# Performance work log

Measured on AMD Instinct MI355X. Metric: run time of the kernel, lower is better.

## Reference

```python
import jax, jax.numpy as jnp
import numpy as np

TEMPERATURE = 0.5
EPS = 1e-12  # torch F.normalize eps


def setup_inputs() -> dict:
    key = jax.random.key(0)
    k1, k2 = jax.random.split(key)
    z_i = jax.random.normal(k1, (32, 128, 128), dtype=jnp.float32)
    z_j = jax.random.normal(k2, (32, 128, 128), dtype=jnp.float32)
    return {"z_i": z_i, "z_j": z_j}


def _l2_normalize(x):
    # matches torch F.normalize(dim=1): x / max(||x||, eps)
    n = jnp.sqrt(jnp.sum(x * x, axis=1, keepdims=True))
    return x / jnp.maximum(n, EPS)


def _off_diagonal(a):
    # rows of a with the diagonal removed, row-major order -> [n, n-1]
    n = a.shape[0]
    return a.reshape(-1)[:-1].reshape(n - 1, n + 1)[:, 1:].reshape(n, n - 1)


def reference(z_i, z_j):
    B, S, D = z_i.shape
    N = B * S
    zi = _l2_normalize(z_i.reshape(N, D))
    zj = _l2_normalize(z_j.reshape(N, D))
    r = jnp.concatenate([zi, zj], axis=0)              # [2N, D]
    sim = r @ r.T                                      # [2N, 2N]
    # positives: off-diagonals at +/-N (unaffected by the diag -inf fill)
    pos = jnp.concatenate([jnp.diagonal(sim, N), jnp.diagonal(sim, -N)])  # [2N]
    # negatives: all non-diagonal entries, row-major (== torch boolean-mask view)
    neg = _off_diagonal(sim)                           # [2N, 2N-1]
    logits = jnp.concatenate([pos[:, None], neg], axis=1) / TEMPERATURE  # [2N, 2N]
    # labels are all 0 -> CE(sum) / 2N == mean of -log_softmax[:, 0]
    loss = -jax.nn.log_softmax(logits, axis=1)[:, 0]
    return jnp.sum(loss) / (2 * N)
```

## Files before the change

### kernel.cpp

```cpp
#include <hip/hip_runtime.h>
#include <hip/hip_bf16.h>
#include <math.h>

#define NPAIR 4096
#define D 128
#define TWO_N 8192
#define NJC 8
#define NPART (NJC * 2)

typedef short bf16x8 __attribute__((ext_vector_type(8)));
typedef float f32x4 __attribute__((ext_vector_type(4)));

__device__ __forceinline__ void async_ld16(void* lds, const void* g) {
    __builtin_amdgcn_global_load_lds(
        (__attribute__((address_space(1))) const unsigned int*)g,
        (__attribute__((address_space(3))) unsigned int*)lds, 16, 0, 0);
}

__device__ inline unsigned short f2bf(float x) {
    union { float f; unsigned u; } v; v.f = x;
    unsigned u = v.u;
    unsigned r = u + 0x7fffu + ((u >> 16) & 1u);
    return (unsigned short)(r >> 16);
}

__global__ __launch_bounds__(256) void norm_kernel(const float* __restrict__ zi,
                                                   const float* __restrict__ zj,
                                                   unsigned int* __restrict__ Rb,
                                                   float* __restrict__ pos,
                                                   float* __restrict__ out) {
    if (blockIdx.x == 0 && threadIdx.x == 0) out[0] = 0.f;
    int k = blockIdx.x * 4 + (threadIdx.x >> 6);
    int t = threadIdx.x & 63;
    const float2 a = *(const float2*)(zi + k * D + 2 * t);
    const float2 b = *(const float2*)(zj + k * D + 2 * t);
    float si = a.x * a.x + a.y * a.y;
    float sj = b.x * b.x + b.y * b.y;
    float dt = a.x * b.x + a.y * b.y;
    #pragma unroll
    for (int m = 1; m < 64; m <<= 1) {
        si += __shfl_xor(si, m, 64);
        sj += __shfl_xor(sj, m, 64);
        dt += __shfl_xor(dt, m, 64);
    }
    float ii = 1.0f / fmaxf(sqrtf(si), 1e-12f);
    float ij = 1.0f / fmaxf(sqrtf(sj), 1e-12f);
    unsigned short b0 = f2bf(a.x * ii), b1 = f2bf(a.y * ii);
    Rb[k * (D / 2) + t] = (unsigned)b0 | ((unsigned)b1 << 16);
    b0 = f2bf(b.x * ij); b1 = f2bf(b.y * ij);
    Rb[(k + NPAIR) * (D / 2) + t] = (unsigned)b0 | ((unsigned)b1 << 16);
    if (t == 0) pos[k] = dt * ii * ij;
}

__global__ __launch_bounds__(256, 2) void simexp_kernel(const uint4* __restrict__ Rb,
                                                        float* __restrict__ rspart) {
    __shared__ uint4 Bs[2][2048];
    const int bi = blockIdx.x >> 3, jc = blockIdx.x & 7;
    const int tid = threadIdx.x;
    const int wave = tid >> 6, lane = tid & 63;
    const int rp = lane & 15, q = lane >> 4;
    const int wr = (wave & 1) * 64;
    const int wc = (wave >> 1) * 64;

    bf16x8 afr[4][4];
    {
        const uint4* Ab = Rb + (bi * 128 + wr + rp) * 16;
        #pragma unroll
        for (int kt = 0; kt < 4; ++kt)
            #pragma unroll
            for (int rt = 0; rt < 4; ++rt)
                afr[kt][rt] = *(const bf16x8*)&Ab[rt * 256 + kt * 4 + q];
    }

    const int rl15 = wave * 4 + q;
    const int laneoff = rl15 * 256 + ((rp ^ rl15) << 4);
    const char* Rbb = (const char*)Rb;

    float rs[16];
    #pragma unroll
    for (int i = 0; i < 16; ++i) rs[i] = 0.f;

    {
        const char* g = Rbb + (jc * 1024) * 256 + laneoff;
        char* l = (char*)&Bs[0][0] + wave * 1024;
        #pragma unroll
        for (int it = 0; it < 8; ++it)
            async_ld16(l + it * 4096, g + it * 4096);
    }

    for (int jt = 0; jt < 8; ++jt) {
        __syncthreads();

        if (jt < 7) {
            const char* g = Rbb + (jc * 1024 + (jt + 1) * 128) * 256 + laneoff;
            char* l = (char*)&Bs[(jt + 1) & 1][0] + wave * 1024;
            #pragma unroll
            for (int it = 0; it < 8; ++it)
                async_ld16(l + it * 4096, g + it * 4096);
        }

        const uint4* B = &Bs[jt & 1][0];
        f32x4 acc[4][4] = {};
        #pragma unroll
        for (int kt = 0; kt < 4; ++kt) {
            const int k = kt * 4 + q;
            bf16x8 bfr[4];
            #pragma unroll
            for (int ct = 0; ct < 4; ++ct) {
                const int crow = wc + ct * 16 + rp;
                bfr[ct] = *(const bf16x8*)&B[crow * 16 + (k ^ rp)];
            }
            #pragma unroll
            for (int rt = 0; rt < 4; ++rt)
                #pragma unroll
                for (int ct = 0; ct < 4; ++ct)
                    acc[rt][ct] = __builtin_amdgcn_mfma_f32_16x16x32_bf16(
                        afr[kt][rt], bfr[ct], acc[rt][ct], 0, 0, 0);
        }

        if (jc * 1024 + jt * 128 == bi * 128) {
            #pragma unroll
            for (int rt = 0; rt < 4; ++rt)
                #pragma unroll
                for (int r = 0; r < 4; ++r) {
                    int ro = wr + q * 4 + rt * 16 + r;
                    float s = 0.f;
                    #pragma unroll
                    for (int ct = 0; ct < 4; ++ct) {
                        int co = wc + ct * 16 + rp;
                        float x = acc[rt][ct][r];
                        float e = __expf(x + x);
                        s += (ro == co) ? 0.f : e;
                    }
                    rs[rt * 4 + r] += s;
                }
        } else {
            #pragma unroll
            for (int rt = 0; rt < 4; ++rt)
                #pragma unroll
                for (int r = 0; r < 4; ++r) {
                    float s = 0.f;
                    #pragma unroll
                    for (int ct = 0; ct < 4; ++ct) {
                        float x = acc[rt][ct][r];
                        s += __expf(x + x);
                    }
                    rs[rt * 4 + r] += s;
                }
        }
    }

    #pragma unroll
    for (int i = 0; i < 16; ++i) {
        float v = rs[i];
        v += __shfl_xor(v, 1, 64);
        v += __shfl_xor(v, 2, 64);
        v += __shfl_xor(v, 4, 64);
        v += __shfl_xor(v, 8, 64);
        rs[i] = v;
    }
    if (rp == 0) {
        const int slab = jc * 2 + (wave >> 1);
        const int rowb = bi * 128 + wr + q * 4;
        #pragma unroll
        for (int rt = 0; rt < 4; ++rt)
            #pragma unroll
            for (int r = 0; r < 4; ++r)
                rspart[slab * TWO_N + rowb + rt * 16 + r] = rs[rt * 4 + r];
    }
}

__global__ __launch_bounds__(256) void finalize_kernel(const float* __restrict__ rspart,
                                                       const float* __restrict__ pos,
                                                       float* __restrict__ out) {
    __shared__ float red[4];
    int tid = threadIdx.x;
    float local = 0.f;
    #pragma unroll
    for (int i = 0; i < 2; ++i) {
        int k = blockIdx.x * 512 + i * 256 + tid;
        float rsum = 0.f;
        #pragma unroll
        for (int p = 0; p < NPART; ++p) rsum += rspart[p * TWO_N + k];
        float ps = pos[k & (NPAIR - 1)];
        float p2 = ps + ps;
        local += logf(rsum + __expf(p2)) - p2;
    }
    #pragma unroll
    for (int m = 1; m < 64; m <<= 1) local += __shfl_xor(local, m, 64);
    if ((tid & 63) == 0) red[tid >> 6] = local;
    __syncthreads();
    if (tid == 0) {
        float s = red[0] + red[1] + red[2] + red[3];
        atomicAdd(out, s * (1.0f / (float)TWO_N));
    }
}

extern "C" void kernel_launch(void* const* d_in, const int* in_sizes, int n_in,
                              void* d_out, int out_size, void* d_ws, size_t ws_size,
                              hipStream_t stream) {
    const float* zi = (const float*)d_in[0];
    const float* zj = (const float*)d_in[1];
    char* ws = (char*)d_ws;
    unsigned int* Rb = (unsigned int*)ws;
    float* rspart = (float*)(ws + 2 * 1024 * 1024);
    float* pos = (float*)(ws + 2 * 1024 * 1024 + 512 * 1024);

    norm_kernel<<<NPAIR / 4, 256, 0, stream>>>(zi, zj, Rb, pos, (float*)d_out);
    simexp_kernel<<<64 * NJC, 256, 0, stream>>>((const uint4*)Rb, rspart);
    finalize_kernel<<<16, 256, 0, stream>>>(rspart, pos, (float*)d_out);
}
```

Measured before the change: 86.26 us.

## Exploit symmetry of similarity matrix with upper-triangular tiles and atomic row sums

```diff
diff --git a/kernel.cpp b/kernel.cpp
--- a/kernel.cpp
+++ b/kernel.cpp
@@ -5,17 +5,9 @@
 #define NPAIR 4096
 #define D 128
 #define TWO_N 8192
-#define NJC 8
-#define NPART (NJC * 2)
 
 typedef short bf16x8 __attribute__((ext_vector_type(8)));
 typedef float f32x4 __attribute__((ext_vector_type(4)));
-
-__device__ __forceinline__ void async_ld16(void* lds, const void* g) {
-    __builtin_amdgcn_global_load_lds(
-        (__attribute__((address_space(1))) const unsigned int*)g,
-        (__attribute__((address_space(3))) unsigned int*)lds, 16, 0, 0);
-}
 
 __device__ inline unsigned short f2bf(float x) {
     union { float f; unsigned u; } v; v.f = x;
@@ -28,8 +20,10 @@
                                                    const float* __restrict__ zj,
                                                    unsigned int* __restrict__ Rb,
                                                    float* __restrict__ pos,
+                                                   float* __restrict__ rowsum,
                                                    float* __restrict__ out) {
-    if (blockIdx.x == 0 && threadIdx.x == 0) out[0] = 0.f;
+    if (threadIdx.x < 8) rowsum[blockIdx.x * 8 + threadIdx.x] = 0.f;
+    if (blockIdx.x == 0 && threadIdx.x == 8) out[0] = 0.f;
     int k = blockIdx.x * 4 + (threadIdx.x >> 6);
     int t = threadIdx.x & 63;
     const float2 a = *(const float2*)(zi + k * D + 2 * t);
@@ -53,9 +47,9 @@
 }
 
 __global__ __launch_bounds__(256, 2) void simexp_kernel(const uint4* __restrict__ Rb,
-                                                        float* __restrict__ rspart) {
-    __shared__ uint4 Bs[2][2048];
-    const int bi = blockIdx.x >> 3, jc = blockIdx.x & 7;
+                                                        float* __restrict__ rowsum) {
+    const int bi = blockIdx.y, bj = blockIdx.x;
+    if (bj < bi) return;
     const int tid = threadIdx.x;
     const int wave = tid >> 6, lane = tid & 63;
     const int rp = lane & 15, q = lane >> 4;
@@ -72,105 +66,80 @@
                 afr[kt][rt] = *(const bf16x8*)&Ab[rt * 256 + kt * 4 + q];
     }
 
-    const int rl15 = wave * 4 + q;
-    const int laneoff = rl15 * 256 + ((rp ^ rl15) << 4);
-    const char* Rbb = (const char*)Rb;
-
-    float rs[16];
+    const uint4* Bb = Rb + (bj * 128 + wc + rp) * 16;
+    f32x4 acc[4][4] = {};
     #pragma unroll
-    for (int i = 0; i < 16; ++i) rs[i] = 0.f;
-
-    {
-        const char* g = Rbb + (jc * 1024) * 256 + laneoff;
-        char* l = (char*)&Bs[0][0] + wave * 1024;
+    for (int kt = 0; kt < 4; ++kt) {
+        bf16x8 bfr[4];
         #pragma unroll
-        for (int it = 0; it < 8; ++it)
-            async_ld16(l + it * 4096, g + it * 4096);
+        for (int ct = 0; ct < 4; ++ct)
+            bfr[ct] = *(const bf16x8*)&Bb[ct * 256 + kt * 4 + q];
+        #pragma unroll
+        for (int rt = 0; rt < 4; ++rt)
+            #pragma unroll
+            for (int ct = 0; ct < 4; ++ct)
+                acc[rt][ct] = __builtin_amdgcn_mfma_f32_16x16x32_bf16(
+                    afr[kt][rt], bfr[ct], acc[rt][ct], 0, 0, 0);
     }
 
-    for (int jt = 0; jt < 8; ++jt) {
-        __syncthreads();
-
-        if (jt < 7) {
-            const char* g = Rbb + (jc * 1024 + (jt + 1) * 128) * 256 + laneoff;
-            char* l = (char*)&Bs[(jt + 1) & 1][0] + wave * 1024;
+    float rsum[16];
+    float csum[4] = {0.f, 0.f, 0.f, 0.f};
+    if (bi == bj) {
+        #pragma unroll
+        for (int rt = 0; rt < 4; ++rt)
             #pragma unroll
-            for (int it = 0; it < 8; ++it)
-                async_ld16(l + it * 4096, g + it * 4096);
-        }
-
-        const uint4* B = &Bs[jt & 1][0];
-        f32x4 acc[4][4] = {};
+            for (int r = 0; r < 4; ++r) {
+                int ro = wr + rt * 16 + q * 4 + r;
+                float s = 0.f;
+                #pragma unroll
+                for (int ct = 0; ct < 4; ++ct) {
+                    int co = wc + ct * 16 + rp;
+                    float x = acc[rt][ct][r];
+                    float e = __expf(x + x);
+                    s += (ro == co) ? 0.f : e;
+                }
+                rsum[rt * 4 + r] = s;
+            }
+    } else {
         #pragma unroll
-        for (int kt = 0; kt < 4; ++kt) {
-            const int k = kt * 4 + q;
-            bf16x8 bfr[4];
+        for (int rt = 0; rt < 4; ++rt)
             #pragma unroll
-            for (int ct = 0; ct < 4; ++ct) {
-                const int crow = wc + ct * 16 + rp;
-                bfr[ct] = *(const bf16x8*)&B[crow * 16 + (k ^ rp)];
+            for (int r = 0; r < 4; ++r) {
+                float s = 0.f;
+                #pragma unroll
+                for (int ct = 0; ct < 4; ++ct) {
+                    float x = acc[rt][ct][r];
+                    float e = __expf(x + x);
+                    s += e;
+                    csum[ct] += e;
+                }
+                rsum[rt * 4 + r] = s;
             }
-            #pragma unroll
-            for (int rt = 0; rt < 4; ++rt)
-                #pragma unroll
-                for (int ct = 0; ct < 4; ++ct)
-                    acc[rt][ct] = __builtin_amdgcn_mfma_f32_16x16x32_bf16(
-                        afr[kt][rt], bfr[ct], acc[rt][ct], 0, 0, 0);
-        }
-
-        if (jc * 1024 + jt * 128 == bi * 128) {
-            #pragma unroll
-            for (int rt = 0; rt < 4; ++rt)
-                #pragma unroll
-                for (int r = 0; r < 4; ++r) {
-                    int ro = wr + q * 4 + rt * 16 + r;
-                    float s = 0.f;
-                    #pragma unroll
-                    for (int ct = 0; ct < 4; ++ct) {
-                        int co = wc + ct * 16 + rp;
-                        float x = acc[rt][ct][r];
-                        float e = __expf(x + x);
-                        s += (ro == co) ? 0.f : e;
-                    }
-                    rs[rt * 4 + r] += s;
-                }
-        } else {
-            #pragma unroll
-            for (int rt = 0; rt < 4; ++rt)
-                #pragma unroll
-                for (int r = 0; r < 4; ++r) {
-                    float s = 0.f;
-                    #pragma unroll
-                    for (int ct = 0; ct < 4; ++ct) {
-                        float x = acc[rt][ct][r];
-                        s += __expf(x + x);
-                    }
-                    rs[rt * 4 + r] += s;
-                }
-        }
     }
 
     #pragma unroll
     for (int i = 0; i < 16; ++i) {
-        float v = rs[i];
+        float v = rsum[i];
         v += __shfl_xor(v, 1, 64);
         v += __shfl_xor(v, 2, 64);
         v += __shfl_xor(v, 4, 64);
         v += __shfl_xor(v, 8, 64);
-        rs[i] = v;
+        if (rp == 0)
+            atomicAdd(&rowsum[bi * 128 + wr + (i >> 2) * 16 + q * 4 + (i & 3)], v);
     }
-    if (rp == 0) {
-        const int slab = jc * 2 + (wave >> 1);
-        const int rowb = bi * 128 + wr + q * 4;
+    if (bi != bj) {
         #pragma unroll
-        for (int rt = 0; rt < 4; ++rt)
-            #pragma unroll
-            for (int r = 0; r < 4; ++r)
-                rspart[slab * TWO_N + rowb + rt * 16 + r] = rs[rt * 4 + r];
+        for (int ct = 0; ct < 4; ++ct) {
+            float v = csum[ct];
+            v += __shfl_xor(v, 16, 64);
+            v += __shfl_xor(v, 32, 64);
+            if (q == 0)
+                atomicAdd(&rowsum[bj * 128 + wc + ct * 16 + rp], v);
+        }
     }
 }
 
-__global__ __launch_bounds__(256) void finalize_kernel(const float* __restrict__ rspart,
+__global__ __launch_bounds__(256) void finalize_kernel(const float* __restrict__ rowsum,
                                                        const float* __restrict__ pos,
                                                        float* __restrict__ out) {
     __shared__ float red[4];
@@ -179,12 +148,9 @@
     #pragma unroll
     for (int i = 0; i < 2; ++i) {
         int k = blockIdx.x * 512 + i * 256 + tid;
-        float rsum = 0.f;
-        #pragma unroll
-        for (int p = 0; p < NPART; ++p) rsum += rspart[p * TWO_N + k];
         float ps = pos[k & (NPAIR - 1)];
         float p2 = ps + ps;
-        local += logf(rsum + __expf(p2)) - p2;
+        local += logf(rowsum[k] + __expf(p2)) - p2;
     }
     #pragma unroll
     for (int m = 1; m < 64; m <<= 1) local += __shfl_xor(local, m, 64);
@@ -203,10 +169,10 @@
     const float* zj = (const float*)d_in[1];
     char* ws = (char*)d_ws;
     unsigned int* Rb = (unsigned int*)ws;
-    float* rspart = (float*)(ws + 2 * 1024 * 1024);
-    float* pos = (float*)(ws + 2 * 1024 * 1024 + 512 * 1024);
+    float* rowsum = (float*)(ws + 2 * 1024 * 1024);
+    float* pos = (float*)(ws + 2 * 1024 * 1024 + 32 * 1024);
 
-    norm_kernel<<<NPAIR / 4, 256, 0, stream>>>(zi, zj, Rb, pos, (float*)d_out);
-    simexp_kernel<<<64 * NJC, 256, 0, stream>>>((const uint4*)Rb, rspart);
-    finalize_kernel<<<16, 256, 0, stream>>>(rspart, pos, (float*)d_out);
+    norm_kernel<<<NPAIR / 4, 256, 0, stream>>>(zi, zj, Rb, pos, rowsum, (float*)d_out);
+    simexp_kernel<<<dim3(64, 64), 256, 0, stream>>>((const uint4*)Rb, rowsum);
+    finalize_kernel<<<16, 256, 0, stream>>>(rowsum, pos, (float*)d_out);
 }
```

Result: slower. 124.3 us (+44.2%).

## Load B fragments directly to registers and fold exp scale into normalization

Applied to the files above, without the earlier changes.

```diff
diff --git a/kernel.cpp b/kernel.cpp
--- a/kernel.cpp
+++ b/kernel.cpp
@@ -7,15 +7,10 @@
 #define TWO_N 8192
 #define NJC 8
 #define NPART (NJC * 2)
+#define ALPHA 1.6986436f
 
 typedef short bf16x8 __attribute__((ext_vector_type(8)));
 typedef float f32x4 __attribute__((ext_vector_type(4)));
-
-__device__ __forceinline__ void async_ld16(void* lds, const void* g) {
-    __builtin_amdgcn_global_load_lds(
-        (__attribute__((address_space(1))) const unsigned int*)g,
-        (__attribute__((address_space(3))) unsigned int*)lds, 16, 0, 0);
-}
 
 __device__ inline unsigned short f2bf(float x) {
     union { float f; unsigned u; } v; v.f = x;
@@ -45,22 +40,22 @@
     }
     float ii = 1.0f / fmaxf(sqrtf(si), 1e-12f);
     float ij = 1.0f / fmaxf(sqrtf(sj), 1e-12f);
+    if (t == 0) pos[k] = dt * ii * ij;
+    ii *= ALPHA; ij *= ALPHA;
     unsigned short b0 = f2bf(a.x * ii), b1 = f2bf(a.y * ii);
     Rb[k * (D / 2) + t] = (unsigned)b0 | ((unsigned)b1 << 16);
     b0 = f2bf(b.x * ij); b1 = f2bf(b.y * ij);
     Rb[(k + NPAIR) * (D / 2) + t] = (unsigned)b0 | ((unsigned)b1 << 16);
-    if (t == 0) pos[k] = dt * ii * ij;
 }
 
 __global__ __launch_bounds__(256, 2) void simexp_kernel(const uint4* __restrict__ Rb,
                                                         float* __restrict__ rspart) {
-    __shared__ uint4 Bs[2][2048];
     const int bi = blockIdx.x >> 3, jc = blockIdx.x & 7;
     const int tid = threadIdx.x;
     const int wave = tid >> 6, lane = tid & 63;
     const int rp = lane & 15, q = lane >> 4;
     const int wr = (wave & 1) * 64;
-    const int wc = (wave >> 1) * 64;
+    const int wc = (wave >> 1) * 32;
 
     bf16x8 afr[4][4];
     {
@@ -72,64 +67,54 @@
                 afr[kt][rt] = *(const bf16x8*)&Ab[rt * 256 + kt * 4 + q];
     }
 
-    const int rl15 = wave * 4 + q;
-    const int laneoff = rl15 * 256 + ((rp ^ rl15) << 4);
-    const char* Rbb = (const char*)Rb;
+    const uint4* Bb = Rb + (jc * 1024 + wc + rp) * 16 + q;
+
+    bf16x8 bfr[2][4][2];
+    #pragma unroll
+    for (int kt = 0; kt < 4; ++kt)
+        #pragma unroll
+        for (int ct = 0; ct < 2; ++ct)
+            bfr[0][kt][ct] = *(const bf16x8*)&Bb[ct * 256 + kt * 4];
 
     float rs[16];
     #pragma unroll
     for (int i = 0; i < 16; ++i) rs[i] = 0.f;
 
-    {
-        const char* g = Rbb + (jc * 1024) * 256 + laneoff;
-        char* l = (char*)&Bs[0][0] + wave * 1024;
-        #pragma unroll
-        for (int it = 0; it < 8; ++it)
-            async_ld16(l + it * 4096, g + it * 4096);
-    }
+    const int diagoff = bi * 128 - jc * 1024;
 
-    for (int jt = 0; jt < 8; ++jt) {
-        __syncthreads();
-
-        if (jt < 7) {
-            const char* g = Rbb + (jc * 1024 + (jt + 1) * 128) * 256 + laneoff;
-            char* l = (char*)&Bs[(jt + 1) & 1][0] + wave * 1024;
+    #pragma unroll
+    for (int jt = 0; jt < 16; ++jt) {
+        const int cur = jt & 1, nxt = cur ^ 1;
+        if (jt < 15) {
             #pragma unroll
-            for (int it = 0; it < 8; ++it)
-                async_ld16(l + it * 4096, g + it * 4096);
+            for (int kt = 0; kt < 4; ++kt)
+                #pragma unroll
+                for (int ct = 0; ct < 2; ++ct)
+                    bfr[nxt][kt][ct] =
+                        *(const bf16x8*)&Bb[(jt + 1) * 1024 + ct * 256 + kt * 4];
         }
 
-        const uint4* B = &Bs[jt & 1][0];
-        f32x4 acc[4][4] = {};
+        f32x4 acc[4][2] = {};
         #pragma unroll
-        for (int kt = 0; kt < 4; ++kt) {
-            const int k = kt * 4 + q;
-            bf16x8 bfr[4];
-            #pragma unroll
-            for (int ct = 0; ct < 4; ++ct) {
-                const int crow = wc + ct * 16 + rp;
-                bfr[ct] = *(const bf16x8*)&B[crow * 16 + (k ^ rp)];
-            }
+        for (int kt = 0; kt < 4; ++kt)
             #pragma unroll
             for (int rt = 0; rt < 4; ++rt)
                 #pragma unroll
-                for (int ct = 0; ct < 4; ++ct)
+                for (int ct = 0; ct < 2; ++ct)
                     acc[rt][ct] = __builtin_amdgcn_mfma_f32_16x16x32_bf16(
-                        afr[kt][rt], bfr[ct], acc[rt][ct], 0, 0, 0);
-        }
+                        afr[kt][rt], bfr[cur][kt][ct], acc[rt][ct], 0, 0, 0);
 
-        if (jc * 1024 + jt * 128 == bi * 128) {
+        if ((unsigned)(jt * 64 - diagoff) < 128u) {
             #pragma unroll
             for (int rt = 0; rt < 4; ++rt)
                 #pragma unroll
                 for (int r = 0; r < 4; ++r) {
-                    int ro = wr + q * 4 + rt * 16 + r;
+                    int ro = wr + rt * 16 + q * 4 + r;
                     float s = 0.f;
                     #pragma unroll
-                    for (int ct = 0; ct < 4; ++ct) {
-                        int co = wc + ct * 16 + rp;
-                        float x = acc[rt][ct][r];
-                        float e = __expf(x + x);
+                    for (int ct = 0; ct < 2; ++ct) {
+                        int co = jt * 64 - diagoff + wc + ct * 16 + rp;
+                        float e = exp2f(acc[rt][ct][r]);
                         s += (ro == co) ? 0.f : e;
                     }
                     rs[rt * 4 + r] += s;
@@ -141,10 +126,8 @@
                 for (int r = 0; r < 4; ++r) {
                     float s = 0.f;
                     #pragma unroll
-                    for (int ct = 0; ct < 4; ++ct) {
-                        float x = acc[rt][ct][r];
-                        s += __expf(x + x);
-                    }
+                    for (int ct = 0; ct < 2; ++ct)
+                        s += exp2f(acc[rt][ct][r]);
                     rs[rt * 4 + r] += s;
                 }
         }
@@ -163,10 +146,8 @@
         const int slab = jc * 2 + (wave >> 1);
         const int rowb = bi * 128 + wr + q * 4;
         #pragma unroll
-        for (int rt = 0; rt < 4; ++rt)
-            #pragma unroll
-            for (int r = 0; r < 4; ++r)
-                rspart[slab * TWO_N + rowb + rt * 16 + r] = rs[rt * 4 + r];
+        for (int i = 0; i < 16; ++i)
+            rspart[slab * TWO_N + rowb + (i >> 2) * 16 + (i & 3)] = rs[i];
     }
 }
 
```

Measured after the change: 97.25 us. 12.7% more time.
